# Kernel tuning notes

Measured on AMD Instinct MI355X. Metric: run time of the kernel, lower is better.

## Reference

```python
import jax, jax.numpy as jnp
import numpy as np

B, N, D, DL, DK, DC = 4, 2048, 1024, 64, 128, 8
G_S, G_2, G_1 = 1.0, 0.5, 0.3
EPS = 1e-6

def _christoffel(dk, dl):
    # Poincare-inspired init: for k < min(dk,dl): row/col k set to 0.01, then -0.01 on the diagonal
    G = np.zeros((dk, dl, dl), np.float32)
    idx = np.arange(dl)
    for k in range(min(dk, dl)):
        G[k, k, :] = 0.01
        G[k, :, k] = 0.01
        G[k, idx, idx] -= 0.01
    return jnp.asarray(G)

def setup_inputs() -> dict:
    key = jax.random.key(0)
    ks = jax.random.split(key, 12)
    inp = {
        'x_query': jax.random.normal(ks[0], (B, D), jnp.float32),
        'z_query': 0.1 * jax.random.normal(ks[1], (B, DL), jnp.float32),
        'x_keys': jax.random.normal(ks[2], (B, N, D), jnp.float32),
        'z_keys': 0.1 * jax.random.normal(ks[3], (B, N, DL), jnp.float32),
        'W_Q': jax.random.normal(ks[4], (DK, D), jnp.float32) / np.sqrt(D),
        'W_Qz': jax.random.normal(ks[5], (DK, DL), jnp.float32) / np.sqrt(DL),
        'W_Qgamma': _christoffel(DK, DL),
        'W_K': jax.random.normal(ks[6], (DK, D), jnp.float32) / np.sqrt(D),
        'W_V': jax.random.normal(ks[7], (DK, D), jnp.float32) / np.sqrt(D),
        'W_O': jax.random.normal(ks[8], (D, DK), jnp.float32) / np.sqrt(DK),
        'W_delta': jax.random.normal(ks[9], (DC, DL), jnp.float32) / np.sqrt(DL),
        'basis_b': 0.01 * jax.random.normal(ks[10], (DC, DK, DK), jnp.float32),
        'basis_e': 0.01 * jax.random.normal(ks[11], (DC, DK, DK), jnp.float32),
        'basis_o': 0.01 * jax.random.normal(jax.random.fold_in(key, 99), (DC, DK, DK), jnp.float32),
        'log_sigma': jnp.asarray(np.log(G_S ** 2), jnp.float32),
    }
    return inp

def reference(x_query, z_query, x_keys, z_keys, W_Q, W_Qz, W_Qgamma,
              W_K, W_V, W_O, W_delta, basis_b, basis_e, basis_o, log_sigma):
    dk = W_Q.shape[0]
    # Christoffel query: linear + position + quadratic form  [B, dk]
    q = x_query @ W_Q.T + z_query @ W_Qz.T \
        + jnp.einsum('aij,bi,bj->ba', W_Qgamma, z_query, z_query)
    k = x_keys @ W_K.T            # [B, N, dk]
    v = x_keys @ W_V.T            # [B, N, dk]
    # Wilson line approx: U = I + sum_r coeff_r * (g * skew(basis_r))
    delta = z_query[:, None, :] - z_keys          # [B, N, DL]
    coeff = delta @ W_delta.T                     # [B, N, DC]
    skew = lambda b: b - jnp.swapaxes(b, -1, -2)
    basis = G_S * skew(basis_b) + G_2 * skew(basis_e) + G_1 * skew(basis_o)  # [DC, dk, dk]
    H = jnp.einsum('bnr,rij->bnij', coeff, basis)  # [B, N, dk, dk]
    kt = k + jnp.einsum('bnij,bnj->bni', H, k)     # (I + H) k
    # Conformal temperature tau = sqrt(dk) / lambda(z)
    r_sq = jnp.clip(jnp.sum(z_query ** 2, axis=-1, keepdims=True), None, 1.0 - EPS)
    lam = 2.0 / (1.0 - r_sq + EPS)                 # [B, 1]
    tau = jnp.sqrt(jnp.float32(dk)) / lam
    scores = jnp.einsum('bd,bnd->bn', q, kt) / tau
    attn = jax.nn.softmax(scores, axis=-1)
    # Area-law screening (level=0 -> sigma_eff = sigma)
    dist_sq = jnp.sum(delta ** 2, axis=-1)         # [B, N]
    area = 0.5 * lam ** 2 * dist_sq
    attn = attn * jnp.exp(-jnp.exp(log_sigma) * area)
    out = jnp.einsum('bn,bnd->bd', attn, v) @ W_O.T  # [B, D]
    return out
```

## Files before the change

### kernel.cpp

```cpp
#include <hip/hip_runtime.h>
#include <math.h>


constexpr int AV_OFF   = 0;
constexpr int SC_OFF   = 36864;
constexpr int WZ_OFF   = 36928;
constexpr int DIST_OFF = 102464;
constexpr int S_OFF    = 110656;
constexpr int AEXP_OFF = 118848;
constexpr int W_OFF    = 127040;
constexpr int XBAR_OFF = 135232;
constexpr int QG_OFF   = 139328;
constexpr int QS_OFF   = 139840;
constexpr int US_OFF   = 140352;
constexpr int Y_OFF    = 144448;
constexpr int WS_FLOATS = 144960;

__device__ __forceinline__ float wave_sum(float v) {
#pragma unroll
  for (int off = 32; off > 0; off >>= 1) v += __shfl_xor(v, off, 64);
  return v;
}

__global__ __launch_bounds__(256) void k_init(
    const float* __restrict__ zq_g, const float* __restrict__ z_keys,
    const float* __restrict__ Wd,   const float* __restrict__ G,
    const float* __restrict__ lsig, float* __restrict__ ws) {
  const int tid = threadIdx.x;
  const int blk = blockIdx.x;

  if (blk < 128) {
    __shared__ float szq[256];
    __shared__ float part[1024];
    __shared__ float red2[256];
    szq[tid] = zq_g[tid];
    __syncthreads();
    const int i = tid >> 2, jc = tid & 3;
    const float* Gp = G + blk * 4096 + i * 64 + jc * 16;
    float pb0 = 0, pb1 = 0, pb2 = 0, pb3 = 0;
#pragma unroll
    for (int k = 0; k < 16; ++k) {
      float g = Gp[k];
      int j = jc * 16 + k;
      pb0 += g * szq[0 * 64 + j];
      pb1 += g * szq[1 * 64 + j];
      pb2 += g * szq[2 * 64 + j];
      pb3 += g * szq[3 * 64 + j];
    }
    part[tid * 4 + 0] = pb0; part[tid * 4 + 1] = pb1;
    part[tid * 4 + 2] = pb2; part[tid * 4 + 3] = pb3;
    __syncthreads();
    if (tid < 64) {
#pragma unroll
      for (int b = 0; b < 4; ++b) {
        float s = part[(tid * 4 + 0) * 4 + b] + part[(tid * 4 + 1) * 4 + b] +
                  part[(tid * 4 + 2) * 4 + b] + part[(tid * 4 + 3) * 4 + b];
        red2[tid * 4 + b] = s * szq[b * 64 + tid];
      }
    }
    __syncthreads();
    if (tid < 4) {
      float s = 0;
      for (int i2 = 0; i2 < 64; ++i2) s += red2[i2 * 4 + tid];
      ws[QG_OFF + tid * 128 + blk] = s;
    }
  } else if (blk < 160) {
    __shared__ float sWd[512];
    __shared__ float szq[256];
    sWd[tid] = Wd[tid];
    sWd[256 + tid] = Wd[256 + tid];
    szq[tid] = zq_g[tid];
    __syncthreads();
    const int bn = (blk - 128) * 256 + tid;
    const int b = bn >> 11;
    const float* zk = z_keys + (size_t)bn * 64;
    const float* zq = szq + b * 64;
    float wz[8] = {0, 0, 0, 0, 0, 0, 0, 0};
    float dist = 0;
    for (int l = 0; l < 64; ++l) {
      float z = zk[l];
      float dz = zq[l] - z;
      dist += dz * dz;
#pragma unroll
      for (int r = 0; r < 8; ++r) wz[r] += sWd[r * 64 + l] * z;
    }
#pragma unroll
    for (int r = 0; r < 8; ++r) ws[WZ_OFF + bn * 8 + r] = wz[r];
    ws[DIST_OFF + bn] = dist;
  } else if (blk == 160) {
    __shared__ float szq[256];
    szq[tid] = zq_g[tid];
    __syncthreads();
    const int b = tid >> 6, l = tid & 63;
    float z = szq[b * 64 + l];
    float r2 = wave_sum(z * z);
    float cz[8];
#pragma unroll
    for (int r = 0; r < 8; ++r) cz[r] = wave_sum(Wd[r * 64 + l] * z);
    if (l == 0) {
      r2 = fminf(r2, 1.0f - 1e-6f);
      float lam = 2.0f / (1.0f - r2 + 1e-6f);
      ws[SC_OFF + b * 16 + 0] = lam / sqrtf(128.0f);
      ws[SC_OFF + b * 16 + 1] = expf(lsig[0]) * 0.5f * lam * lam;
#pragma unroll
      for (int r = 0; r < 8; ++r) ws[SC_OFF + b * 16 + 2 + r] = cz[r];
    }
  } else {
    const int b = blk - 161;
    for (int i = tid; i < 1024; i += 256) ws[XBAR_OFF + b * 1024 + i] = 0.0f;
  }
}

__global__ __launch_bounds__(256) void k_q(
    const float* __restrict__ xq_g, const float* __restrict__ zq_g,
    const float* __restrict__ WQ,   const float* __restrict__ WQz,
    float* __restrict__ ws) {
  const int b = blockIdx.x, as_ = blockIdx.y, tid = threadIdx.x;
  __shared__ __align__(16) float xqs[1024];
  __shared__ float zq[64];
  __shared__ float part[256];
  for (int i = tid; i < 1024; i += 256) xqs[i] = xq_g[b * 1024 + i];
  if (tid < 64) zq[tid] = zq_g[b * 64 + tid];
  __syncthreads();

  const int a_loc = tid >> 4, seg = tid & 15;
  const int a = as_ * 16 + a_loc;
  const float4* wq4 = (const float4*)(WQ + a * 1024 + seg * 64);
  const float4* xs4 = (const float4*)(xqs + seg * 64);
  float p = 0;
#pragma unroll
  for (int c = 0; c < 16; ++c) {
    float4 w = wq4[c], x = xs4[c];
    p += w.x * x.x + w.y * x.y + w.z * x.z + w.w * x.w;
  }
#pragma unroll
  for (int c = 0; c < 4; ++c)
    p += WQz[a * 64 + seg * 4 + c] * zq[seg * 4 + c];
  part[tid] = p;
  __syncthreads();
  if (tid < 16) {
    float s = 0;
#pragma unroll
    for (int h = 0; h < 16; ++h) s += part[tid * 16 + h];
    const int aa = as_ * 16 + tid;
    ws[QS_OFF + b * 128 + aa] = s + ws[QG_OFF + b * 128 + aa];
  }
}

__global__ __launch_bounds__(256) void k_u(
    const float* __restrict__ bb, const float* __restrict__ be,
    const float* __restrict__ bo, float* __restrict__ ws) {
  const int r = blockIdx.x, tid = threadIdx.x;
  __shared__ float tmp[128 * 129];
  __shared__ float sq[512];
  __shared__ float red[1024];
  for (int o = tid; o < 512; o += 256) sq[o] = ws[QS_OFF + o];
  __syncthreads();

  const int j = tid & 127, half = tid >> 7;
  float acc[4] = {0, 0, 0, 0};
  const float* arrs[3] = {bb, be, bo};
  const float wgt[3] = {1.0f, 0.5f, 0.3f};

  for (int arr = 0; arr < 3; ++arr) {
    const float4* src = (const float4*)(arrs[arr] + r * 16384);
    for (int idx = tid; idx < 4096; idx += 256) {
      float4 v = src[idx];
      const int i = idx >> 5, col = (idx & 31) * 4;
      float* dst = tmp + i * 129 + col;
      dst[0] = v.x; dst[1] = v.y; dst[2] = v.z; dst[3] = v.w;
    }
    __syncthreads();
    const float w = wgt[arr];
    for (int ii = 0; ii < 64; ++ii) {
      const int i = half * 64 + ii;
      const float d = w * (tmp[i * 129 + j] - tmp[j * 129 + i]);
#pragma unroll
      for (int b = 0; b < 4; ++b) acc[b] += d * sq[b * 128 + i];
    }
    __syncthreads();
  }
#pragma unroll
  for (int b = 0; b < 4; ++b) red[half * 512 + b * 128 + j] = acc[b];
  __syncthreads();
  for (int o = tid; o < 512; o += 256) {
    const int b = o >> 7, jj = o & 127;
    ws[US_OFF + b * 1024 + r * 128 + jj] = red[o] + red[512 + o];
  }
}

__global__ __launch_bounds__(256) void k_av(
    const float* __restrict__ WK, float* __restrict__ ws) {
  const int b = blockIdx.x, dbase = blockIdx.y * 64, tid = threadIdx.x;
  __shared__ float qu[1152];
  __shared__ float part[2304];
  __shared__ float fin[576];
  __shared__ float czq[8];
  for (int o = tid; o < 1152; o += 256)
    qu[o] = (o < 128) ? ws[QS_OFF + b * 128 + o]
                      : ws[US_OFF + b * 1024 + (o - 128)];
  if (tid < 8) czq[tid] = ws[SC_OFF + b * 16 + 2 + tid];
  __syncthreads();

  const int kq = tid >> 6, dloc = tid & 63;
  float acc[9];
#pragma unroll
  for (int jj = 0; jj < 9; ++jj) acc[jj] = 0;
  const float* wkp = WK + dbase + dloc;
#pragma unroll 4
  for (int k = kq * 32; k < kq * 32 + 32; ++k) {
    const float wk = wkp[k * 1024];
#pragma unroll
    for (int jj = 0; jj < 9; ++jj) acc[jj] += qu[jj * 128 + k] * wk;
  }
#pragma unroll
  for (int jj = 0; jj < 9; ++jj) part[kq * 576 + jj * 64 + dloc] = acc[jj];
  __syncthreads();
  for (int o = tid; o < 576; o += 256)
    fin[o] = part[o] + part[576 + o] + part[1152 + o] + part[1728 + o];
  __syncthreads();
  float* av = ws + AV_OFF + b * 9216;
  for (int o = tid; o < 576; o += 256) {
    const int jj = o >> 6, dl = o & 63;
    float val = fin[o];
    if (jj == 0) {
#pragma unroll
      for (int rr = 0; rr < 8; ++rr) val += czq[rr] * fin[(1 + rr) * 64 + dl];
    }
    av[jj * 1024 + dbase + dl] = val;
  }
}

__global__ __launch_bounds__(256) void k2_scores(
    const float* __restrict__ x_keys, float* __restrict__ ws) {
  __shared__ __align__(16) float sav[9216];
  __shared__ float s_sc[2];
  const int tid = threadIdx.x;
  const int b = blockIdx.y;
  const float* avg = ws + AV_OFF + b * 9216;
  for (int i = tid * 4; i < 9216; i += 1024)
    *(float4*)(sav + i) = *(const float4*)(avg + i);
  if (tid < 2) s_sc[tid] = ws[SC_OFF + b * 16 + tid];
  __syncthreads();

  const int wave = tid >> 6, lane = tid & 63;
  const int nbase = blockIdx.x * 16 + wave * 4;
  const float* xb = x_keys + ((size_t)(b * 2048 + nbase)) * 1024;

  float acc[9][4];
#pragma unroll
  for (int j = 0; j < 9; ++j)
#pragma unroll
    for (int p = 0; p < 4; ++p) acc[j][p] = 0;

#pragma unroll
  for (int c = 0; c < 4; ++c) {
    const int off = c * 256 + lane * 4;
    float4 xv[4];
#pragma unroll
    for (int p = 0; p < 4; ++p)
      xv[p] = *(const float4*)(xb + p * 1024 + off);
#pragma unroll
    for (int j = 0; j < 9; ++j) {
      float4 a = *(const float4*)(sav + j * 1024 + off);
#pragma unroll
      for (int p = 0; p < 4; ++p)
        acc[j][p] += a.x * xv[p].x + a.y * xv[p].y + a.z * xv[p].z + a.w * xv[p].w;
    }
  }
#pragma unroll
  for (int j = 0; j < 9; ++j)
#pragma unroll
    for (int p = 0; p < 4; ++p) acc[j][p] = wave_sum(acc[j][p]);

  if (lane == 0) {
    const float it = s_sc[0], sc = s_sc[1];
    for (int p = 0; p < 4; ++p) {
      const int bn = b * 2048 + nbase + p;
      const float* wz = ws + WZ_OFF + bn * 8;
      float s = acc[0][p];
#pragma unroll
      for (int r = 0; r < 8; ++r) s -= wz[r] * acc[1 + r][p];
      ws[S_OFF + bn] = s * it;
      ws[AEXP_OFF + bn] = sc * ws[DIST_OFF + bn];
    }
  }
}

__global__ __launch_bounds__(256) void k3_softmax(float* __restrict__ ws) {
  const int b = blockIdx.x, tid = threadIdx.x;
  __shared__ float red[256];
  float sv[8];
  float vmax = -1e30f;
#pragma unroll
  for (int i = 0; i < 8; ++i) {
    sv[i] = ws[S_OFF + b * 2048 + i * 256 + tid];
    vmax = fmaxf(vmax, sv[i]);
  }
  red[tid] = vmax;
  __syncthreads();
  for (int s = 128; s > 0; s >>= 1) {
    if (tid < s) red[tid] = fmaxf(red[tid], red[tid + s]);
    __syncthreads();
  }
  const float m = red[0];
  __syncthreads();
  float lsum = 0;
#pragma unroll
  for (int i = 0; i < 8; ++i) lsum += expf(sv[i] - m);
  red[tid] = lsum;
  __syncthreads();
  for (int s = 128; s > 0; s >>= 1) {
    if (tid < s) red[tid] += red[tid + s];
    __syncthreads();
  }
  const float rl = 1.0f / red[0];
#pragma unroll
  for (int i = 0; i < 8; ++i) {
    const int idx = b * 2048 + i * 256 + tid;
    ws[W_OFF + idx] = expf(sv[i] - m - ws[AEXP_OFF + idx]) * rl;
  }
}

__global__ __launch_bounds__(256) void k4_xbar(
    const float* __restrict__ x_keys, float* __restrict__ ws) {
  const int tid = threadIdx.x;
  const int nt = blockIdx.x, dsl = blockIdx.y, b = blockIdx.z;
  __shared__ float sw[256];
  const int n0 = nt * 256;
  sw[tid] = ws[W_OFF + b * 2048 + n0 + tid];
  __syncthreads();
  const int d = dsl * 256 + tid;
  const float* xb = x_keys + ((size_t)(b * 2048 + n0)) * 1024 + d;
  float a0 = 0, a1 = 0, a2 = 0, a3 = 0;
  for (int n = 0; n < 256; n += 4) {
    a0 += sw[n + 0] * xb[(size_t)(n + 0) * 1024];
    a1 += sw[n + 1] * xb[(size_t)(n + 1) * 1024];
    a2 += sw[n + 2] * xb[(size_t)(n + 2) * 1024];
    a3 += sw[n + 3] * xb[(size_t)(n + 3) * 1024];
  }
  atomicAdd(&ws[XBAR_OFF + b * 1024 + d], (a0 + a1) + (a2 + a3));
}

__global__ __launch_bounds__(256) void k5a_y(
    const float* __restrict__ WV, float* __restrict__ ws) {
  const int b = blockIdx.x, sl = blockIdx.y, tid = threadIdx.x;
  __shared__ __align__(16) float sx[1024];
  __shared__ float part[256];
  for (int i = tid; i < 1024; i += 256) sx[i] = ws[XBAR_OFF + b * 1024 + i];
  __syncthreads();
  const int dk_loc = tid >> 4, seg = tid & 15;
  const int dk = sl * 16 + dk_loc;
  const float4* wv4 = (const float4*)(WV + dk * 1024 + seg * 64);
  const float4* xs4 = (const float4*)(sx + seg * 64);
  float p = 0;
#pragma unroll
  for (int c = 0; c < 16; ++c) {
    float4 w = wv4[c], x = xs4[c];
    p += w.x * x.x + w.y * x.y + w.z * x.z + w.w * x.w;
  }
  part[tid] = p;
  __syncthreads();
  if (tid < 16) {
    float s = 0;
#pragma unroll
    for (int h = 0; h < 16; ++h) s += part[tid * 16 + h];
    ws[Y_OFF + b * 128 + sl * 16 + tid] = s;
  }
}

__global__ __launch_bounds__(256) void k5b_out(
    const float* __restrict__ WO, const float* __restrict__ ws,
    float* __restrict__ out) {
  const int b = blockIdx.x, dsl = blockIdx.y, tid = threadIdx.x;
  __shared__ float sy[128];
  if (tid < 128) sy[tid] = ws[Y_OFF + b * 128 + tid];
  __syncthreads();
  const int d = dsl * 256 + tid;
  const float4* wo4 = (const float4*)(WO + d * 128);
  float acc = 0;
#pragma unroll
  for (int c = 0; c < 32; ++c) {
    float4 w = wo4[c];
    acc += w.x * sy[c * 4 + 0] + w.y * sy[c * 4 + 1] +
           w.z * sy[c * 4 + 2] + w.w * sy[c * 4 + 3];
  }
  out[b * 1024 + d] = acc;
}

extern "C" void kernel_launch(void* const* d_in, const int* in_sizes, int n_in,
                              void* d_out, int out_size, void* d_ws,
                              size_t ws_size, hipStream_t stream) {
  const float* xq  = (const float*)d_in[0];
  const float* zq  = (const float*)d_in[1];
  const float* xk  = (const float*)d_in[2];
  const float* zk  = (const float*)d_in[3];
  const float* WQ  = (const float*)d_in[4];
  const float* WQz = (const float*)d_in[5];
  const float* G   = (const float*)d_in[6];
  const float* WK  = (const float*)d_in[7];
  const float* WV  = (const float*)d_in[8];
  const float* WO  = (const float*)d_in[9];
  const float* Wd  = (const float*)d_in[10];
  const float* bb  = (const float*)d_in[11];
  const float* be  = (const float*)d_in[12];
  const float* bo  = (const float*)d_in[13];
  const float* ls  = (const float*)d_in[14];
  float* ws  = (float*)d_ws;
  float* out = (float*)d_out;
  if (ws_size < (size_t)WS_FLOATS * sizeof(float)) return;

  hipLaunchKernelGGL(k_init, dim3(165), dim3(256), 0, stream,
                     zq, zk, Wd, G, ls, ws);
  hipLaunchKernelGGL(k_q, dim3(4, 8), dim3(256), 0, stream,
                     xq, zq, WQ, WQz, ws);
  hipLaunchKernelGGL(k_u, dim3(8), dim3(256), 0, stream, bb, be, bo, ws);
  hipLaunchKernelGGL(k_av, dim3(4, 16), dim3(256), 0, stream, WK, ws);
  hipLaunchKernelGGL(k2_scores, dim3(128, 4), dim3(256), 0, stream, xk, ws);
  hipLaunchKernelGGL(k3_softmax, dim3(4), dim3(256), 0, stream, ws);
  hipLaunchKernelGGL(k4_xbar, dim3(8, 4, 4), dim3(256), 0, stream, xk, ws);
  hipLaunchKernelGGL(k5a_y, dim3(4, 8), dim3(256), 0, stream, WV, ws);
  hipLaunchKernelGGL(k5b_out, dim3(4, 4), dim3(256), 0, stream, WO, ws, out);
}
```

Baseline: 167.8 us.

## Fuse pipeline into four kernels with split-softmax partial weighted key sums

The nine-kernel pipeline becomes four. Query, Christoffel and key-side prep are merged into one front kernel, and the Wilson-line basis combination is merged with the W_K projection. The scores kernel now also computes per-tile max/sum statistics and screened partial weighted sums of x_keys while the tile is hot. A final kernel rescales and merges the partials, then applies W_V and W_O. This removes the second full pass over x_keys, the atomics and several launches, at the cost of a larger workspace of partial sums that the last kernel reduces through only four blocks.

```diff
diff --git a/kernel.cpp b/kernel.cpp
--- a/kernel.cpp
+++ b/kernel.cpp
@@ -2,19 +2,14 @@
 #include <math.h>
 
 
-constexpr int AV_OFF   = 0;
-constexpr int SC_OFF   = 36864;
-constexpr int WZ_OFF   = 36928;
-constexpr int DIST_OFF = 102464;
-constexpr int S_OFF    = 110656;
-constexpr int AEXP_OFF = 118848;
-constexpr int W_OFF    = 127040;
-constexpr int XBAR_OFF = 135232;
-constexpr int QG_OFF   = 139328;
-constexpr int QS_OFF   = 139840;
-constexpr int US_OFF   = 140352;
-constexpr int Y_OFF    = 144448;
-constexpr int WS_FLOATS = 144960;
+constexpr int SC_OFF   = 0;
+constexpr int WZ_OFF   = 64;
+constexpr int DIST_OFF = 65600;
+constexpr int QS_OFF   = 73792;
+constexpr int AV_OFF   = 74304;
+constexpr int ML_OFF   = 111168;
+constexpr int PX_OFF   = 112192;
+constexpr int WS_FLOATS = 636480;
 
 __device__ __forceinline__ float wave_sum(float v) {
 #pragma unroll
@@ -22,230 +17,182 @@
   return v;
 }
 
-__global__ __launch_bounds__(256) void k_init(
-    const float* __restrict__ zq_g, const float* __restrict__ z_keys,
-    const float* __restrict__ Wd,   const float* __restrict__ G,
-    const float* __restrict__ lsig, float* __restrict__ ws) {
+__global__ __launch_bounds__(256) void k_front(
+    const float* __restrict__ xq, const float* __restrict__ zq,
+    const float* __restrict__ zk, const float* __restrict__ WQ,
+    const float* __restrict__ WQz, const float* __restrict__ G,
+    const float* __restrict__ Wd, const float* __restrict__ lsig,
+    float* __restrict__ ws) {
   const int tid = threadIdx.x;
-  const int blk = blockIdx.x;
-
-  if (blk < 128) {
-    __shared__ float szq[256];
-    __shared__ float part[1024];
-    __shared__ float red2[256];
-    szq[tid] = zq_g[tid];
-    __syncthreads();
-    const int i = tid >> 2, jc = tid & 3;
-    const float* Gp = G + blk * 4096 + i * 64 + jc * 16;
-    float pb0 = 0, pb1 = 0, pb2 = 0, pb3 = 0;
-#pragma unroll
-    for (int k = 0; k < 16; ++k) {
-      float g = Gp[k];
-      int j = jc * 16 + k;
-      pb0 += g * szq[0 * 64 + j];
-      pb1 += g * szq[1 * 64 + j];
-      pb2 += g * szq[2 * 64 + j];
-      pb3 += g * szq[3 * 64 + j];
-    }
-    part[tid * 4 + 0] = pb0; part[tid * 4 + 1] = pb1;
-    part[tid * 4 + 2] = pb2; part[tid * 4 + 3] = pb3;
-    __syncthreads();
-    if (tid < 64) {
-#pragma unroll
-      for (int b = 0; b < 4; ++b) {
-        float s = part[(tid * 4 + 0) * 4 + b] + part[(tid * 4 + 1) * 4 + b] +
-                  part[(tid * 4 + 2) * 4 + b] + part[(tid * 4 + 3) * 4 + b];
-        red2[tid * 4 + b] = s * szq[b * 64 + tid];
+  const int bid = blockIdx.x;
+  __shared__ __align__(16) float smem[1344];
+
+  if (bid < 32) {
+    float* xqs  = smem;
+    float* zqs  = smem + 1024;
+    float* part = smem + 1088;
+    const int b = bid >> 3, as_ = bid & 7;
+    for (int i = tid; i < 1024; i += 256) xqs[i] = xq[b * 1024 + i];
+    if (tid < 64) zqs[tid] = zq[b * 64 + tid];
+    __syncthreads();
+    const int a_loc = tid >> 4, seg = tid & 15;
+    const int a = as_ * 16 + a_loc;
+    const float4* wq4 = (const float4*)(WQ + a * 1024 + seg * 64);
+    const float4* xs4 = (const float4*)(xqs + seg * 64);
+    float p = 0;
+#pragma unroll
+    for (int c = 0; c < 16; ++c) {
+      float4 w = wq4[c], x = xs4[c];
+      p += w.x * x.x + w.y * x.y + w.z * x.z + w.w * x.w;
+    }
+#pragma unroll
+    for (int c = 0; c < 4; ++c)
+      p += WQz[a * 64 + seg * 4 + c] * zqs[seg * 4 + c];
+    const float4* zq4 = (const float4*)zqs;
+#pragma unroll
+    for (int ii = 0; ii < 4; ++ii) {
+      const int i = seg * 4 + ii;
+      const float4* g4 = (const float4*)(G + a * 4096 + i * 64);
+      float gi = 0;
+#pragma unroll
+      for (int c = 0; c < 16; ++c) {
+        float4 g = g4[c], z = zq4[c];
+        gi += g.x * z.x + g.y * z.y + g.z * z.z + g.w * z.w;
       }
-    }
-    __syncthreads();
-    if (tid < 4) {
+      p += gi * zqs[i];
+    }
+    part[tid] = p;
+    __syncthreads();
+    if (tid < 16) {
       float s = 0;
-      for (int i2 = 0; i2 < 64; ++i2) s += red2[i2 * 4 + tid];
-      ws[QG_OFF + tid * 128 + blk] = s;
-    }
-  } else if (blk < 160) {
-    __shared__ float sWd[512];
-    __shared__ float szq[256];
+#pragma unroll
+      for (int h = 0; h < 16; ++h) s += part[tid * 16 + h];
+      ws[QS_OFF + b * 128 + as_ * 16 + tid] = s;
+    }
+  } else if (bid < 64) {
+    float* sWd = smem;
+    float* szq = smem + 512;
     sWd[tid] = Wd[tid];
     sWd[256 + tid] = Wd[256 + tid];
-    szq[tid] = zq_g[tid];
-    __syncthreads();
-    const int bn = (blk - 128) * 256 + tid;
+    szq[tid] = zq[tid];
+    __syncthreads();
+    const int bn = (bid - 32) * 256 + tid;
     const int b = bn >> 11;
-    const float* zk = z_keys + (size_t)bn * 64;
-    const float* zq = szq + b * 64;
-    float wz[8] = {0, 0, 0, 0, 0, 0, 0, 0};
+    const float4* zk4 = (const float4*)(zk + (size_t)bn * 64);
+    const float* zqb = szq + b * 64;
+    float wzv[8] = {0, 0, 0, 0, 0, 0, 0, 0};
     float dist = 0;
-    for (int l = 0; l < 64; ++l) {
-      float z = zk[l];
-      float dz = zq[l] - z;
-      dist += dz * dz;
-#pragma unroll
-      for (int r = 0; r < 8; ++r) wz[r] += sWd[r * 64 + l] * z;
-    }
-#pragma unroll
-    for (int r = 0; r < 8; ++r) ws[WZ_OFF + bn * 8 + r] = wz[r];
+#pragma unroll
+    for (int c = 0; c < 16; ++c) {
+      const float4 z = zk4[c];
+      const int l = c * 4;
+      float d0 = zqb[l + 0] - z.x, d1 = zqb[l + 1] - z.y;
+      float d2 = zqb[l + 2] - z.z, d3 = zqb[l + 3] - z.w;
+      dist += d0 * d0 + d1 * d1 + d2 * d2 + d3 * d3;
+#pragma unroll
+      for (int r = 0; r < 8; ++r)
+        wzv[r] += sWd[r * 64 + l] * z.x + sWd[r * 64 + l + 1] * z.y +
+                  sWd[r * 64 + l + 2] * z.z + sWd[r * 64 + l + 3] * z.w;
+    }
+#pragma unroll
+    for (int r = 0; r < 8; ++r) ws[WZ_OFF + bn * 8 + r] = wzv[r];
     ws[DIST_OFF + bn] = dist;
-  } else if (blk == 160) {
-    __shared__ float szq[256];
-    szq[tid] = zq_g[tid];
+  } else {
+    float* szq = smem;
+    szq[tid] = zq[tid];
     __syncthreads();
     const int b = tid >> 6, l = tid & 63;
-    float z = szq[b * 64 + l];
+    const float z = szq[b * 64 + l];
     float r2 = wave_sum(z * z);
     float cz[8];
 #pragma unroll
     for (int r = 0; r < 8; ++r) cz[r] = wave_sum(Wd[r * 64 + l] * z);
     if (l == 0) {
       r2 = fminf(r2, 1.0f - 1e-6f);
-      float lam = 2.0f / (1.0f - r2 + 1e-6f);
+      const float lam = 2.0f / (1.0f - r2 + 1e-6f);
       ws[SC_OFF + b * 16 + 0] = lam / sqrtf(128.0f);
       ws[SC_OFF + b * 16 + 1] = expf(lsig[0]) * 0.5f * lam * lam;
 #pragma unroll
       for (int r = 0; r < 8; ++r) ws[SC_OFF + b * 16 + 2 + r] = cz[r];
     }
-  } else {
-    const int b = blk - 161;
-    for (int i = tid; i < 1024; i += 256) ws[XBAR_OFF + b * 1024 + i] = 0.0f;
-  }
-}
-
-__global__ __launch_bounds__(256) void k_q(
-    const float* __restrict__ xq_g, const float* __restrict__ zq_g,
-    const float* __restrict__ WQ,   const float* __restrict__ WQz,
+  }
+}
+
+__global__ __launch_bounds__(256) void k_uav(
+    const float* __restrict__ bb, const float* __restrict__ be,
+    const float* __restrict__ bo, const float* __restrict__ WK,
     float* __restrict__ ws) {
-  const int b = blockIdx.x, as_ = blockIdx.y, tid = threadIdx.x;
-  __shared__ __align__(16) float xqs[1024];
-  __shared__ float zq[64];
-  __shared__ float part[256];
-  for (int i = tid; i < 1024; i += 256) xqs[i] = xq_g[b * 1024 + i];
-  if (tid < 64) zq[tid] = zq_g[b * 64 + tid];
-  __syncthreads();
-
-  const int a_loc = tid >> 4, seg = tid & 15;
-  const int a = as_ * 16 + a_loc;
-  const float4* wq4 = (const float4*)(WQ + a * 1024 + seg * 64);
-  const float4* xs4 = (const float4*)(xqs + seg * 64);
-  float p = 0;
-#pragma unroll
-  for (int c = 0; c < 16; ++c) {
-    float4 w = wq4[c], x = xs4[c];
-    p += w.x * x.x + w.y * x.y + w.z * x.z + w.w * x.w;
-  }
-#pragma unroll
-  for (int c = 0; c < 4; ++c)
-    p += WQz[a * 64 + seg * 4 + c] * zq[seg * 4 + c];
-  part[tid] = p;
-  __syncthreads();
-  if (tid < 16) {
-    float s = 0;
-#pragma unroll
-    for (int h = 0; h < 16; ++h) s += part[tid * 16 + h];
-    const int aa = as_ * 16 + tid;
-    ws[QS_OFF + b * 128 + aa] = s + ws[QG_OFF + b * 128 + aa];
-  }
-}
-
-__global__ __launch_bounds__(256) void k_u(
-    const float* __restrict__ bb, const float* __restrict__ be,
-    const float* __restrict__ bo, float* __restrict__ ws) {
-  const int r = blockIdx.x, tid = threadIdx.x;
+  const int jj = blockIdx.x, dsl = blockIdx.y, tid = threadIdx.x;
   __shared__ float tmp[128 * 129];
   __shared__ float sq[512];
   __shared__ float red[1024];
+  __shared__ float su[512];
   for (int o = tid; o < 512; o += 256) sq[o] = ws[QS_OFF + o];
   __syncthreads();
 
-  const int j = tid & 127, half = tid >> 7;
-  float acc[4] = {0, 0, 0, 0};
-  const float* arrs[3] = {bb, be, bo};
-  const float wgt[3] = {1.0f, 0.5f, 0.3f};
-
-  for (int arr = 0; arr < 3; ++arr) {
-    const float4* src = (const float4*)(arrs[arr] + r * 16384);
+  if (jj == 0) {
+    for (int o = tid; o < 512; o += 256) su[o] = sq[o];
+  } else {
+    const int r = jj - 1;
+    const float4* b4 = (const float4*)(bb + r * 16384);
+    const float4* e4 = (const float4*)(be + r * 16384);
+    const float4* o4 = (const float4*)(bo + r * 16384);
     for (int idx = tid; idx < 4096; idx += 256) {
-      float4 v = src[idx];
+      const float4 vb = b4[idx], ve = e4[idx], vo = o4[idx];
       const int i = idx >> 5, col = (idx & 31) * 4;
       float* dst = tmp + i * 129 + col;
-      dst[0] = v.x; dst[1] = v.y; dst[2] = v.z; dst[3] = v.w;
-    }
-    __syncthreads();
-    const float w = wgt[arr];
+      dst[0] = vb.x + 0.5f * ve.x + 0.3f * vo.x;
+      dst[1] = vb.y + 0.5f * ve.y + 0.3f * vo.y;
+      dst[2] = vb.z + 0.5f * ve.z + 0.3f * vo.z;
+      dst[3] = vb.w + 0.5f * ve.w + 0.3f * vo.w;
+    }
+    __syncthreads();
+    const int j = tid & 127, h = tid >> 7;
+    float a[4] = {0, 0, 0, 0};
     for (int ii = 0; ii < 64; ++ii) {
-      const int i = half * 64 + ii;
-      const float d = w * (tmp[i * 129 + j] - tmp[j * 129 + i]);
-#pragma unroll
-      for (int b = 0; b < 4; ++b) acc[b] += d * sq[b * 128 + i];
-    }
-    __syncthreads();
-  }
-#pragma unroll
-  for (int b = 0; b < 4; ++b) red[half * 512 + b * 128 + j] = acc[b];
-  __syncthreads();
-  for (int o = tid; o < 512; o += 256) {
-    const int b = o >> 7, jj = o & 127;
-    ws[US_OFF + b * 1024 + r * 128 + jj] = red[o] + red[512 + o];
-  }
-}
-
-__global__ __launch_bounds__(256) void k_av(
-    const float* __restrict__ WK, float* __restrict__ ws) {
-  const int b = blockIdx.x, dbase = blockIdx.y * 64, tid = threadIdx.x;
-  __shared__ float qu[1152];
-  __shared__ float part[2304];
-  __shared__ float fin[576];
-  __shared__ float czq[8];
-  for (int o = tid; o < 1152; o += 256)
-    qu[o] = (o < 128) ? ws[QS_OFF + b * 128 + o]
-                      : ws[US_OFF + b * 1024 + (o - 128)];
-  if (tid < 8) czq[tid] = ws[SC_OFF + b * 16 + 2 + tid];
-  __syncthreads();
-
-  const int kq = tid >> 6, dloc = tid & 63;
-  float acc[9];
-#pragma unroll
-  for (int jj = 0; jj < 9; ++jj) acc[jj] = 0;
-  const float* wkp = WK + dbase + dloc;
-#pragma unroll 4
-  for (int k = kq * 32; k < kq * 32 + 32; ++k) {
-    const float wk = wkp[k * 1024];
-#pragma unroll
-    for (int jj = 0; jj < 9; ++jj) acc[jj] += qu[jj * 128 + k] * wk;
-  }
-#pragma unroll
-  for (int jj = 0; jj < 9; ++jj) part[kq * 576 + jj * 64 + dloc] = acc[jj];
-  __syncthreads();
-  for (int o = tid; o < 576; o += 256)
-    fin[o] = part[o] + part[576 + o] + part[1152 + o] + part[1728 + o];
-  __syncthreads();
-  float* av = ws + AV_OFF + b * 9216;
-  for (int o = tid; o < 576; o += 256) {
-    const int jj = o >> 6, dl = o & 63;
-    float val = fin[o];
-    if (jj == 0) {
-#pragma unroll
-      for (int rr = 0; rr < 8; ++rr) val += czq[rr] * fin[(1 + rr) * 64 + dl];
-    }
-    av[jj * 1024 + dbase + dl] = val;
-  }
-}
-
-__global__ __launch_bounds__(256) void k2_scores(
-    const float* __restrict__ x_keys, float* __restrict__ ws) {
+      const int i = h * 64 + ii;
+      const float d = tmp[i * 129 + j] - tmp[j * 129 + i];
+#pragma unroll
+      for (int b = 0; b < 4; ++b) a[b] += d * sq[b * 128 + i];
+    }
+#pragma unroll
+    for (int b = 0; b < 4; ++b) red[h * 512 + b * 128 + j] = a[b];
+    __syncthreads();
+    for (int o = tid; o < 512; o += 256) su[o] = red[o] + red[512 + o];
+  }
+  __syncthreads();
+
+  const int dbase = dsl * 256;
+  for (int o = tid; o < 1024; o += 256) {
+    const int b = o >> 8, dl = o & 255;
+    const float* wk = WK + dbase + dl;
+    const float* ub = su + b * 128;
+    float acc = 0;
+#pragma unroll 8
+    for (int k = 0; k < 128; ++k) acc += ub[k] * wk[(size_t)k * 1024];
+    ws[AV_OFF + b * 9216 + jj * 1024 + dbase + dl] = acc;
+  }
+}
+
+__global__ __launch_bounds__(256) void k_scpx(
+    const float* __restrict__ xk, float* __restrict__ ws) {
   __shared__ __align__(16) float sav[9216];
-  __shared__ float s_sc[2];
+  __shared__ float pw[4096];
+  __shared__ float ssc[10];
+  __shared__ float sw16[16];
+  __shared__ float wexp[16];
+  __shared__ float wscr[16];
   const int tid = threadIdx.x;
-  const int b = blockIdx.y;
+  const int b = blockIdx.y, jb = blockIdx.x;
   const float* avg = ws + AV_OFF + b * 9216;
   for (int i = tid * 4; i < 9216; i += 1024)
     *(float4*)(sav + i) = *(const float4*)(avg + i);
-  if (tid < 2) s_sc[tid] = ws[SC_OFF + b * 16 + tid];
+  if (tid < 10) ssc[tid] = ws[SC_OFF + b * 16 + tid];
   __syncthreads();
 
   const int wave = tid >> 6, lane = tid & 63;
-  const int nbase = blockIdx.x * 16 + wave * 4;
-  const float* xb = x_keys + ((size_t)(b * 2048 + nbase)) * 1024;
+  const int nbase = jb * 16 + wave * 4;
+  const float* xb = xk + ((size_t)(b * 2048 + nbase)) * 1024;
 
   float acc[9][4];
 #pragma unroll
@@ -259,7 +206,7 @@
     float4 xv[4];
 #pragma unroll
     for (int p = 0; p < 4; ++p)
-      xv[p] = *(const float4*)(xb + p * 1024 + off);
+      xv[p] = *(const float4*)(xb + (size_t)p * 1024 + off);
 #pragma unroll
     for (int j = 0; j < 9; ++j) {
       float4 a = *(const float4*)(sav + j * 1024 + off);
@@ -274,118 +221,106 @@
     for (int p = 0; p < 4; ++p) acc[j][p] = wave_sum(acc[j][p]);
 
   if (lane == 0) {
-    const float it = s_sc[0], sc = s_sc[1];
+    const float it = ssc[0];
     for (int p = 0; p < 4; ++p) {
       const int bn = b * 2048 + nbase + p;
-      const float* wz = ws + WZ_OFF + bn * 8;
+      const float* wzp = ws + WZ_OFF + bn * 8;
       float s = acc[0][p];
 #pragma unroll
-      for (int r = 0; r < 8; ++r) s -= wz[r] * acc[1 + r][p];
-      ws[S_OFF + bn] = s * it;
-      ws[AEXP_OFF + bn] = sc * ws[DIST_OFF + bn];
-    }
-  }
-}
-
-__global__ __launch_bounds__(256) void k3_softmax(float* __restrict__ ws) {
+      for (int r = 0; r < 8; ++r) s += (ssc[2 + r] - wzp[r]) * acc[1 + r][p];
+      sw16[wave * 4 + p] = s * it;
+    }
+  }
+  __syncthreads();
+
+  if (tid < 16) {
+    float mj = sw16[0];
+#pragma unroll
+    for (int t = 1; t < 16; ++t) mj = fmaxf(mj, sw16[t]);
+    const int n0 = jb * 16;
+    wexp[tid] = expf(sw16[tid] - mj);
+    wscr[tid] = expf(sw16[tid] - mj -
+                     ssc[1] * ws[DIST_OFF + b * 2048 + n0 + tid]);
+  }
+  __syncthreads();
+  if (tid == 0) {
+    float mj = sw16[0];
+#pragma unroll
+    for (int t = 1; t < 16; ++t) mj = fmaxf(mj, sw16[t]);
+    float l = 0;
+#pragma unroll
+    for (int t = 0; t < 16; ++t) l += wexp[t];
+    ws[ML_OFF + (b * 128 + jb) * 2 + 0] = mj;
+    ws[ML_OFF + (b * 128 + jb) * 2 + 1] = l;
+  }
+
+  {
+    const float w0 = wscr[wave * 4 + 0], w1 = wscr[wave * 4 + 1];
+    const float w2 = wscr[wave * 4 + 2], w3 = wscr[wave * 4 + 3];
+    float* pwv = pw + wave * 1024;
+    for (int d = lane; d < 1024; d += 64)
+      pwv[d] = w0 * xb[d] + w1 * xb[1024 + d] +
+               w2 * xb[2048 + d] + w3 * xb[3072 + d];
+  }
+  __syncthreads();
+  float* px = ws + PX_OFF + ((size_t)(b * 128 + jb)) * 1024;
+  for (int o = tid; o < 1024; o += 256)
+    px[o] = pw[o] + pw[1024 + o] + pw[2048 + o] + pw[3072 + o];
+}
+
+__global__ __launch_bounds__(256) void k_fix_epi(
+    const float* __restrict__ WV, const float* __restrict__ WO,
+    const float* __restrict__ ws, float* __restrict__ out) {
   const int b = blockIdx.x, tid = threadIdx.x;
-  __shared__ float red[256];
-  float sv[8];
-  float vmax = -1e30f;
-#pragma unroll
-  for (int i = 0; i < 8; ++i) {
-    sv[i] = ws[S_OFF + b * 2048 + i * 256 + tid];
-    vmax = fmaxf(vmax, sv[i]);
-  }
-  red[tid] = vmax;
-  __syncthreads();
-  for (int s = 128; s > 0; s >>= 1) {
-    if (tid < s) red[tid] = fmaxf(red[tid], red[tid + s]);
-    __syncthreads();
-  }
-  const float m = red[0];
-  __syncthreads();
-  float lsum = 0;
-#pragma unroll
-  for (int i = 0; i < 8; ++i) lsum += expf(sv[i] - m);
-  red[tid] = lsum;
-  __syncthreads();
-  for (int s = 128; s > 0; s >>= 1) {
-    if (tid < s) red[tid] += red[tid + s];
-    __syncthreads();
-  }
-  const float rl = 1.0f / red[0];
-#pragma unroll
-  for (int i = 0; i < 8; ++i) {
-    const int idx = b * 2048 + i * 256 + tid;
-    ws[W_OFF + idx] = expf(sv[i] - m - ws[AEXP_OFF + idx]) * rl;
-  }
-}
-
-__global__ __launch_bounds__(256) void k4_xbar(
-    const float* __restrict__ x_keys, float* __restrict__ ws) {
-  const int tid = threadIdx.x;
-  const int nt = blockIdx.x, dsl = blockIdx.y, b = blockIdx.z;
-  __shared__ float sw[256];
-  const int n0 = nt * 256;
-  sw[tid] = ws[W_OFF + b * 2048 + n0 + tid];
-  __syncthreads();
-  const int d = dsl * 256 + tid;
-  const float* xb = x_keys + ((size_t)(b * 2048 + n0)) * 1024 + d;
-  float a0 = 0, a1 = 0, a2 = 0, a3 = 0;
-  for (int n = 0; n < 256; n += 4) {
-    a0 += sw[n + 0] * xb[(size_t)(n + 0) * 1024];
-    a1 += sw[n + 1] * xb[(size_t)(n + 1) * 1024];
-    a2 += sw[n + 2] * xb[(size_t)(n + 2) * 1024];
-    a3 += sw[n + 3] * xb[(size_t)(n + 3) * 1024];
-  }
-  atomicAdd(&ws[XBAR_OFF + b * 1024 + d], (a0 + a1) + (a2 + a3));
-}
-
-__global__ __launch_bounds__(256) void k5a_y(
-    const float* __restrict__ WV, float* __restrict__ ws) {
-  const int b = blockIdx.x, sl = blockIdx.y, tid = threadIdx.x;
-  __shared__ __align__(16) float sx[1024];
-  __shared__ float part[256];
-  for (int i = tid; i < 1024; i += 256) sx[i] = ws[XBAR_OFF + b * 1024 + i];
-  __syncthreads();
-  const int dk_loc = tid >> 4, seg = tid & 15;
-  const int dk = sl * 16 + dk_loc;
-  const float4* wv4 = (const float4*)(WV + dk * 1024 + seg * 64);
-  const float4* xs4 = (const float4*)(sx + seg * 64);
+  __shared__ float sml[256];
+  __shared__ float scj[128];
+  __shared__ __align__(16) float sxb[1024];
+  __shared__ float sy[128];
+  __shared__ float sL[1];
+  sml[tid] = ws[ML_OFF + b * 256 + tid];
+  __syncthreads();
+  float M = -3.0e38f;
+  for (int j2 = 0; j2 < 256; j2 += 2) M = fmaxf(M, sml[j2]);
+  if (tid < 128) scj[tid] = expf(sml[2 * tid] - M);
+  __syncthreads();
+  if (tid == 0) {
+    float L = 0;
+    for (int j = 0; j < 128; ++j) L += scj[j] * sml[2 * j + 1];
+    sL[0] = 1.0f / L;
+  }
+  __syncthreads();
+  const float rL = sL[0];
+  const float* px = ws + PX_OFF + (size_t)b * 131072;
+  for (int o = tid; o < 1024; o += 256) {
+    float acc = 0;
+#pragma unroll 8
+    for (int j = 0; j < 128; ++j) acc += scj[j] * px[(size_t)j * 1024 + o];
+    sxb[o] = acc * rL;
+  }
+  __syncthreads();
+  const int dk = tid >> 1, h = tid & 1;
+  const float4* wv4 = (const float4*)(WV + dk * 1024 + h * 512);
+  const float4* sx4 = (const float4*)(sxb + h * 512);
   float p = 0;
-#pragma unroll
-  for (int c = 0; c < 16; ++c) {
-    float4 w = wv4[c], x = xs4[c];
+#pragma unroll 16
+  for (int c = 0; c < 128; ++c) {
+    float4 w = wv4[c], x = sx4[c];
     p += w.x * x.x + w.y * x.y + w.z * x.z + w.w * x.w;
   }
-  part[tid] = p;
-  __syncthreads();
-  if (tid < 16) {
-    float s = 0;
-#pragma unroll
-    for (int h = 0; h < 16; ++h) s += part[tid * 16 + h];
-    ws[Y_OFF + b * 128 + sl * 16 + tid] = s;
-  }
-}
-
-__global__ __launch_bounds__(256) void k5b_out(
-    const float* __restrict__ WO, const float* __restrict__ ws,
-    float* __restrict__ out) {
-  const int b = blockIdx.x, dsl = blockIdx.y, tid = threadIdx.x;
-  __shared__ float sy[128];
-  if (tid < 128) sy[tid] = ws[Y_OFF + b * 128 + tid];
-  __syncthreads();
-  const int d = dsl * 256 + tid;
-  const float4* wo4 = (const float4*)(WO + d * 128);
-  float acc = 0;
-#pragma unroll
-  for (int c = 0; c < 32; ++c) {
-    float4 w = wo4[c];
-    acc += w.x * sy[c * 4 + 0] + w.y * sy[c * 4 + 1] +
-           w.z * sy[c * 4 + 2] + w.w * sy[c * 4 + 3];
-  }
-  out[b * 1024 + d] = acc;
+  p += __shfl_xor(p, 1, 64);
+  if (h == 0) sy[dk] = p;
+  __syncthreads();
+  for (int dd = tid; dd < 1024; dd += 256) {
+    const float4* wo4 = (const float4*)(WO + dd * 128);
+    float acc = 0;
+#pragma unroll
+    for (int c = 0; c < 32; ++c) {
+      float4 w = wo4[c];
+      acc += w.x * sy[c * 4 + 0] + w.y * sy[c * 4 + 1] +
+             w.z * sy[c * 4 + 2] + w.w * sy[c * 4 + 3];
+    }
+    out[b * 1024 + dd] = acc;
+  }
 }
 
 extern "C" void kernel_launch(void* const* d_in, const int* in_sizes, int n_in,
@@ -410,15 +345,11 @@
   float* out = (float*)d_out;
   if (ws_size < (size_t)WS_FLOATS * sizeof(float)) return;
 
-  hipLaunchKernelGGL(k_init, dim3(165), dim3(256), 0, stream,
-                     zq, zk, Wd, G, ls, ws);
-  hipLaunchKernelGGL(k_q, dim3(4, 8), dim3(256), 0, stream,
-                     xq, zq, WQ, WQz, ws);
-  hipLaunchKernelGGL(k_u, dim3(8), dim3(256), 0, stream, bb, be, bo, ws);
-  hipLaunchKernelGGL(k_av, dim3(4, 16), dim3(256), 0, stream, WK, ws);
-  hipLaunchKernelGGL(k2_scores, dim3(128, 4), dim3(256), 0, stream, xk, ws);
-  hipLaunchKernelGGL(k3_softmax, dim3(4), dim3(256), 0, stream, ws);
-  hipLaunchKernelGGL(k4_xbar, dim3(8, 4, 4), dim3(256), 0, stream, xk, ws);
-  hipLaunchKernelGGL(k5a_y, dim3(4, 8), dim3(256), 0, stream, WV, ws);
-  hipLaunchKernelGGL(k5b_out, dim3(4, 4), dim3(256), 0, stream, WO, ws, out);
-}
+  hipLaunchKernelGGL(k_front, dim3(65), dim3(256), 0, stream,
+                     xq, zq, zk, WQ, WQz, G, Wd, ls, ws);
+  hipLaunchKernelGGL(k_uav, dim3(9, 4), dim3(256), 0, stream,
+                     bb, be, bo, WK, ws);
+  hipLaunchKernelGGL(k_scpx, dim3(128, 4), dim3(256), 0, stream, xk, ws);
+  hipLaunchKernelGGL(k_fix_epi, dim3(4), dim3(256), 0, stream,
+                     WV, WO, ws, out);
+}
```

New measurement: 209.5 us. 1.25x slower.
